# Kernel optimization log

Measured on AMD Instinct MI355X. Metric: run time of the kernel, lower is better.

## Reference

```python
import jax, jax.numpy as jnp
import numpy as np

VOCAB = 32000
EMBED = 1024
HIDDEN = 1024
BATCH = 256
SEQ = 1024


def setup_inputs() -> dict:
    key = jax.random.key(0)
    k1, k2, k3, k4, k5, k6 = jax.random.split(key, 6)
    x = jax.random.randint(k1, (BATCH, SEQ), 0, VOCAB)
    emb = jax.random.normal(k2, (VOCAB, EMBED), dtype=jnp.float32) * 0.02
    # nn.Linear(input_dim, hidden_dim): weight [out, in], bias [out]
    Wi = jax.random.normal(k3, (HIDDEN, EMBED), dtype=jnp.float32) * (1.0 / np.sqrt(EMBED))
    bi = jax.random.normal(k4, (HIDDEN,), dtype=jnp.float32) * 0.01
    Wh = jax.random.normal(k5, (HIDDEN, HIDDEN), dtype=jnp.float32) * (1.0 / np.sqrt(HIDDEN))
    bh = jax.random.normal(k6, (HIDDEN,), dtype=jnp.float32) * 0.01
    return {"x": x, "emb": emb, "Wi": Wi, "bi": bi, "Wh": Wh, "bh": bh}


def reference(x, emb, Wi, bi, Wh, bh):
    # Embed all tokens up front: [B, T, E]
    ex = emb[x]
    # Precompute input projection for every step (batched GEMM): [B, T, H]
    xi = jnp.einsum('bte,he->bth', ex, Wi) + bi
    h0 = jnp.zeros((x.shape[0], Wh.shape[0]), dtype=emb.dtype)

    def step(h, xi_t):  # xi_t: [B, H]
        h_new = jnp.tanh(xi_t + h @ Wh.T + bh)
        return h_new, None

    h_final, _ = jax.lax.scan(step, h0, jnp.swapaxes(xi, 0, 1))  # scan over T
    return h_final  # [B, H]
```

## Files before the change

### kernel.cpp

```cpp
#include <hip/hip_runtime.h>
#include <cmath>

#define BATCHN 256
#define SEQT   1024
#define EMBED  1024
#define HID    1024
#define VOCABN 32000

typedef __attribute__((ext_vector_type(8))) _Float16 half8;
typedef __attribute__((ext_vector_type(4))) _Float16 half4;
typedef __attribute__((ext_vector_type(4))) float    float4v;
typedef __attribute__((ext_vector_type(4))) unsigned int uint4v;

#define LOSCALE 4096.0f
#define LOINV   (1.0f/4096.0f)

union FU16 { _Float16 f; unsigned short u; };
__device__ inline unsigned short f16bits(_Float16 f){ FU16 t; t.f=f; return t.u; }
__device__ inline _Float16 bits16(unsigned short u){ FU16 t; t.u=u; return t.f; }

__device__ inline void async16(const void* g, void* l) {
  __builtin_amdgcn_global_load_lds(
      (const __attribute__((address_space(1))) void*)g,
      (__attribute__((address_space(3))) void*)l, 16, 0, 0);
}

__global__ void convert_f32_f16(const float* __restrict__ in,
                                _Float16* __restrict__ out, int n) {
  int i = (blockIdx.x * blockDim.x + threadIdx.x) * 4;
  if (i + 3 < n) {
    float4v v = *reinterpret_cast<const float4v*>(in + i);
    half4 o;
#pragma unroll
    for (int j = 0; j < 4; ++j) o[j] = (_Float16)v[j];
    *reinterpret_cast<half4*>(out + i) = o;
  }
}

__global__ void split_f32_f16(const float* __restrict__ in,
                              _Float16* __restrict__ hi,
                              _Float16* __restrict__ lo, int n) {
  int i = (blockIdx.x * blockDim.x + threadIdx.x) * 4;
  if (i + 3 < n) {
    float4v v = *reinterpret_cast<const float4v*>(in + i);
    half4 h, l;
#pragma unroll
    for (int j = 0; j < 4; ++j) {
      h[j] = (_Float16)v[j];
      l[j] = (_Float16)((v[j] - (float)h[j]) * LOSCALE);
    }
    *reinterpret_cast<half4*>(hi + i) = h;
    *reinterpret_cast<half4*>(lo + i) = l;
  }
}

__global__ __launch_bounds__(256, 2) void gemm_xi(
    const _Float16* __restrict__ embh,
    const _Float16* __restrict__ Wih,
    const int* __restrict__ x,
    const float* __restrict__ bi,
    _Float16* __restrict__ xi,
    int t0, int Tc)
{
  __shared__ __align__(16) _Float16 As[128 * 64];
  __shared__ __align__(16) _Float16 Bs[128 * 64];
  __shared__ __align__(16) _Float16 stage[128 * 132];
  __shared__ int toks[128];

  const int tid  = threadIdx.x;
  const int wid  = tid >> 6, lane = tid & 63;
  const int nt   = blockIdx.x & 7, mt = blockIdx.x >> 3;
  const int m0   = mt * 128, n0 = nt * 128;

  if (tid < 128) {
    int m  = m0 + tid;
    int tl = m >> 8;
    int b  = m & 255;
    toks[tid] = x[b * SEQT + t0 + tl];
  }
  __syncthreads();

  const _Float16* aptr[4];
  const _Float16* bptr[4];
  int ldsoff[4];
#pragma unroll
  for (int i = 0; i < 4; ++i) {
    int idx = i * 256 + tid;
    int row = idx >> 3, kc = idx & 7;
    aptr[i]   = embh + (size_t)toks[row] * 1024 + kc * 8;
    bptr[i]   = Wih + ((size_t)(n0 + row) << 10) + kc * 8;
    ldsoff[i] = idx * 8;
  }

  float4v acc[4][4] = {};
  const int wm = wid & 1, wn = wid >> 1;
  const int cn = lane & 15, kg = lane >> 4;

  for (int k0 = 0; k0 < 1024; k0 += 64) {
#pragma unroll
    for (int i = 0; i < 4; ++i) {
      async16(aptr[i] + k0, &As[ldsoff[i]]);
      async16(bptr[i] + k0, &Bs[ldsoff[i]]);
    }
    __syncthreads();

    half8 a[4][2], b[4][2];
#pragma unroll
    for (int mf = 0; mf < 4; ++mf)
#pragma unroll
      for (int kf = 0; kf < 2; ++kf)
        a[mf][kf] = *reinterpret_cast<const half8*>(
            &As[(wm * 64 + mf * 16 + cn) * 64 + kf * 32 + kg * 8]);
#pragma unroll
    for (int nf = 0; nf < 4; ++nf)
#pragma unroll
      for (int kf = 0; kf < 2; ++kf)
        b[nf][kf] = *reinterpret_cast<const half8*>(
            &Bs[(wn * 64 + nf * 16 + cn) * 64 + kf * 32 + kg * 8]);

#pragma unroll
    for (int mf = 0; mf < 4; ++mf)
#pragma unroll
      for (int nf = 0; nf < 4; ++nf)
#pragma unroll
        for (int kf = 0; kf < 2; ++kf)
          acc[mf][nf] = __builtin_amdgcn_mfma_f32_16x16x32_f16(
              a[mf][kf], b[nf][kf], acc[mf][nf], 0, 0, 0);
    __syncthreads();
  }

#pragma unroll
  for (int nf = 0; nf < 4; ++nf) {
    int n = wn * 64 + nf * 16 + cn;
    float biv = bi[n0 + n];
#pragma unroll
    for (int mf = 0; mf < 4; ++mf) {
#pragma unroll
      for (int j = 0; j < 4; ++j) {
        int m = wm * 64 + mf * 16 + kg * 4 + j;
        stage[m * 132 + n] = (_Float16)(acc[mf][nf][j] + biv);
      }
    }
  }
  __syncthreads();
#pragma unroll
  for (int p = 0; p < 8; ++p) {
    int chunk = p * 256 + tid;
    int r = chunk >> 4, cc = chunk & 15;
    half4 v0 = *reinterpret_cast<const half4*>(stage + r * 132 + cc * 8);
    half4 v1 = *reinterpret_cast<const half4*>(stage + r * 132 + cc * 8 + 4);
    half8 o;
#pragma unroll
    for (int e = 0; e < 4; ++e) { o[e] = v0[e]; o[4 + e] = v1[e]; }
    int m  = m0 + r;
    int tt = m >> 8, b = m & 255;
    int n  = n0 + cc * 8;
    size_t addr = ((size_t)(tt * 256 + (b >> 4) * 16 + (n >> 6)) << 10)
                + (size_t)((b & 15) * 64 + (n & 63));
    *reinterpret_cast<half8*>(xi + addr) = o;
  }
}

__global__ __launch_bounds__(256, 1) void rnn_scan(
    const _Float16* __restrict__ Whig,
    const _Float16* __restrict__ Wlog,
    const float* __restrict__ bh,
    const _Float16* __restrict__ xi,
    float* __restrict__ hstate,
    float* __restrict__ out,
    _Float16* __restrict__ hexHiA,
    _Float16* __restrict__ hexLoA,
    _Float16* __restrict__ hexHiB,
    _Float16* __restrict__ hexLoB,
    int* __restrict__ bar,
    int t0, int Tc)
{
  __shared__ __align__(16) _Float16 Ahi[16 * 1024];
  __shared__ __align__(16) _Float16 Alo[16 * 1024];
  __shared__ __align__(16) float    part[4 * 64 * 20];

  const int tid  = threadIdx.x;
  const int wv   = tid >> 6, lane = tid & 63;
  const int cn   = lane & 15, kg = lane >> 4;
  const int gb   = blockIdx.x >> 4;
  const int gc   = blockIdx.x & 15;
  const int r0   = gb * 16;
  const int wcol = gc * 64 + wv * 16 + cn;

  half8 whi[32], wlo[32];
#pragma unroll
  for (int c = 0; c < 4; ++c)
#pragma unroll
    for (int kkl = 0; kkl < 8; ++kkl) {
      int col = gc * 64 + c * 16 + cn;
      int k   = (wv * 8 + kkl) * 32 + kg * 8;
      whi[c * 8 + kkl] = *reinterpret_cast<const half8*>(Whig + ((size_t)col << 10) + k);
      wlo[c * 8 + kkl] = *reinterpret_cast<const half8*>(Wlog + ((size_t)col << 10) + k);
    }
  const float bhv = bh[wcol];

  const size_t xibase = ((size_t)(gb * 16 + gc) << 10) + wv * 16 + cn;

  if (t0 == 0) {
#pragma unroll
    for (int p = 0; p < 8; ++p) {
      int idx = p * 256 + tid, row = idx >> 7, cc = idx & 127;
      int bo = (((row << 11) + cc * 16) ^ ((row & 7) << 4));
      half8 z = {0, 0, 0, 0, 0, 0, 0, 0};
      *reinterpret_cast<half8*>(reinterpret_cast<char*>(Ahi) + bo) = z;
      *reinterpret_cast<half8*>(reinterpret_cast<char*>(Alo) + bo) = z;
    }
  } else {
#pragma unroll
    for (int p = 0; p < 8; ++p) {
      int idx = p * 256 + tid, row = idx >> 7, cc = idx & 127;
      const float* hp = hstate + (((size_t)(r0 + row)) << 10) + cc * 8;
      half8 vh, vl;
#pragma unroll
      for (int e = 0; e < 8; ++e) {
        float f = hp[e];
        _Float16 hi = (_Float16)f;
        vh[e] = hi;
        vl[e] = (_Float16)((f - (float)hi) * LOSCALE);
      }
      int bo = (((row << 11) + cc * 16) ^ ((row & 7) << 4));
      *reinterpret_cast<half8*>(reinterpret_cast<char*>(Ahi) + bo) = vh;
      *reinterpret_cast<half8*>(reinterpret_cast<char*>(Alo) + bo) = vl;
    }
  }
  __syncthreads();

  unsigned int xr[4];
#pragma unroll
  for (int j = 0; j < 4; ++j) {
    unsigned long long ap = (unsigned long long)(xi + xibase + (size_t)(kg * 4 + j) * 64);
    asm volatile("global_load_ushort %0, %1, off" : "=v"(xr[j]) : "v"(ap) : "memory");
  }

  uint4v u1h[4], u1l[4];

#define MFMA_Q(K0, K1)                                                          \
  _Pragma("unroll")                                                             \
  for (int kkl = (K0); kkl < (K1); ++kkl) {                                     \
    int ab = (((cn << 11) + (wv * 8 + kkl) * 64 + kg * 16) ^ ((cn & 7) << 4));  \
    half8 ah = *reinterpret_cast<const half8*>(reinterpret_cast<const char*>(Ahi) + ab); \
    half8 al = *reinterpret_cast<const half8*>(reinterpret_cast<const char*>(Alo) + ab); \
    _Pragma("unroll")                                                           \
    for (int c = 0; c < 4; ++c) {                                               \
      asm("v_mfma_f32_16x16x32_f16 %0, %1, %2, %0" : "+v"(ac1[c]) : "v"(ah), "a"(whi[c * 8 + kkl])); \
      asm("v_mfma_f32_16x16x32_f16 %0, %1, %2, %0" : "+v"(ac2[c]) : "v"(al), "a"(whi[c * 8 + kkl])); \
      asm("v_mfma_f32_16x16x32_f16 %0, %1, %2, %0" : "+v"(ac3[c]) : "v"(ah), "a"(wlo[c * 8 + kkl])); \
    }                                                                           \
  }

  for (int tt = 0; tt < Tc; ++tt) {
    float4v ac1[4] = {}, ac2[4] = {}, ac3[4] = {};

    MFMA_Q(0, 4)

    if (tt != 0) {
      asm volatile("s_waitcnt vmcnt(0)" ::: "memory");
      __builtin_amdgcn_sched_barrier(0);
#pragma unroll
      for (int p = 0; p < 4; ++p) {
        int gcbl = 2 + (p >> 1), ch = (p & 1) * 64 + lane;
        int rowl = ch >> 3, c8 = ch & 7;
        int gcb  = wv * 4 + gcbl;
        int bo = (((rowl << 11) + gcb * 128 + c8 * 16) ^ ((rowl & 7) << 4));
        *reinterpret_cast<uint4v*>(reinterpret_cast<char*>(Ahi) + bo) = u1h[p];
        *reinterpret_cast<uint4v*>(reinterpret_cast<char*>(Alo) + bo) = u1l[p];
      }
      asm volatile("s_waitcnt lgkmcnt(0)" ::: "memory");
      __builtin_amdgcn_sched_barrier(0);
    }

    MFMA_Q(4, 8)
    asm volatile("s_nop 7\n\ts_nop 7");

#pragma unroll
    for (int c = 0; c < 4; ++c) {
      float4v pv;
#pragma unroll
      for (int j = 0; j < 4; ++j)
        pv[j] = ac1[c][j] + (ac2[c][j] + ac3[c][j]) * LOINV;
      *reinterpret_cast<float4v*>(&part[(wv * 64 + c * 16 + cn) * 20 + kg * 4]) = pv;
    }
    __syncthreads();

    float4v vs = {};
#pragma unroll
    for (int w = 0; w < 4; ++w) {
      float4v pw = *reinterpret_cast<const float4v*>(
          &part[(w * 64 + wv * 16 + cn) * 20 + kg * 4]);
#pragma unroll
      for (int j = 0; j < 4; ++j) vs[j] += pw[j];
    }
    asm volatile("s_waitcnt vmcnt(0)" ::: "memory");

    const int tglob = t0 + tt;
    const int par = (tt + 1) & 1;
    _Float16* WHi = par ? hexHiA : hexHiB;
    _Float16* WLo = par ? hexLoA : hexLoB;
#pragma unroll
    for (int j = 0; j < 4; ++j) {
      int rowl = kg * 4 + j;
      int row  = r0 + rowl;
      float v = vs[j] + bhv + (float)bits16((unsigned short)xr[j]);
      float ex = __expf(2.0f * v);
      float h  = 1.0f - 2.0f / (ex + 1.0f);
      if (tt < Tc - 1) {
        FU16 thi, tlo;
        thi.f = (_Float16)h;
        tlo.f = (_Float16)((h - (float)thi.f) * LOSCALE);
        size_t off = (((size_t)(gb * 16 + gc)) << 10) + rowl * 64 + wv * 16 + cn;
        asm volatile("global_store_short %0, %1, off sc0 sc1"
                     :: "v"((unsigned long long)(WHi + off)), "v"((unsigned int)thi.u) : "memory");
        asm volatile("global_store_short %0, %1, off sc0 sc1"
                     :: "v"((unsigned long long)(WLo + off)), "v"((unsigned int)tlo.u) : "memory");
      }
      if (tglob == SEQT - 1) out[(((size_t)row) << 10) + wcol] = h;
      else if (tt == Tc - 1) hstate[(((size_t)row) << 10) + wcol] = h;
    }
    if (tt == Tc - 1) break;

    asm volatile("s_waitcnt vmcnt(0)" ::: "memory");
    __builtin_amdgcn_s_barrier();
    const int target = tt + 1;
    if (tid == 0)
      asm volatile("global_store_dword %0, %1, off sc0 sc1"
                   :: "v"((unsigned long long)(bar + (gb * 16 + gc) * 32)),
                      "v"(target) : "memory");

#pragma unroll
    for (int j = 0; j < 4; ++j) {
      unsigned long long ap = (unsigned long long)
          (xi + xibase + (((size_t)(tt + 1)) << 18) + (size_t)(kg * 4 + j) * 64);
      asm volatile("global_load_ushort %0, %1, off" : "=v"(xr[j]) : "v"(ap) : "memory");
    }

    if (tid < 16) {
      const int* fp = bar + (gb * 16 + tid) * 32;
      for (;;) {
        int v;
        asm volatile("global_load_dword %0, %1, off sc0 sc1\n\t"
                     "s_waitcnt vmcnt(0)"
                     : "=v"(v) : "v"((unsigned long long)fp) : "memory");
        if (v >= target) break;
        __builtin_amdgcn_s_sleep(1);
      }
    }
    __builtin_amdgcn_s_barrier();

    const _Float16* SHi = par ? hexHiA : hexHiB;
    const _Float16* SLo = par ? hexLoA : hexLoB;
    uint4v u0h[4], u0l[4];
#pragma unroll
    for (int p = 0; p < 4; ++p) {
      int gcbl = p >> 1, ch = (p & 1) * 64 + lane;
      int rowl = ch >> 3, c8 = ch & 7;
      int gcb  = wv * 4 + gcbl;
      size_t off = (((size_t)(gb * 16 + gcb)) << 10) + rowl * 64 + c8 * 8;
      asm volatile("global_load_dwordx4 %0, %1, off sc0 sc1"
                   : "=v"(u0h[p]) : "v"((unsigned long long)(SHi + off)) : "memory");
      asm volatile("global_load_dwordx4 %0, %1, off sc0 sc1"
                   : "=v"(u0l[p]) : "v"((unsigned long long)(SLo + off)) : "memory");
    }
#pragma unroll
    for (int p = 0; p < 4; ++p) {
      int gcbl = 2 + (p >> 1), ch = (p & 1) * 64 + lane;
      int rowl = ch >> 3, c8 = ch & 7;
      int gcb  = wv * 4 + gcbl;
      size_t off = (((size_t)(gb * 16 + gcb)) << 10) + rowl * 64 + c8 * 8;
      asm volatile("global_load_dwordx4 %0, %1, off sc0 sc1"
                   : "=v"(u1h[p]) : "v"((unsigned long long)(SHi + off)) : "memory");
      asm volatile("global_load_dwordx4 %0, %1, off sc0 sc1"
                   : "=v"(u1l[p]) : "v"((unsigned long long)(SLo + off)) : "memory");
    }
    asm volatile("s_waitcnt vmcnt(8)" ::: "memory");
    __builtin_amdgcn_sched_barrier(0);
#pragma unroll
    for (int p = 0; p < 4; ++p) {
      int gcbl = p >> 1, ch = (p & 1) * 64 + lane;
      int rowl = ch >> 3, c8 = ch & 7;
      int gcb  = wv * 4 + gcbl;
      int bo = (((rowl << 11) + gcb * 128 + c8 * 16) ^ ((rowl & 7) << 4));
      *reinterpret_cast<uint4v*>(reinterpret_cast<char*>(Ahi) + bo) = u0h[p];
      *reinterpret_cast<uint4v*>(reinterpret_cast<char*>(Alo) + bo) = u0l[p];
    }
    asm volatile("s_waitcnt lgkmcnt(0)" ::: "memory");
    __builtin_amdgcn_sched_barrier(0);
  }
#undef MFMA_Q
}

extern "C" void kernel_launch(void* const* d_in, const int* in_sizes, int n_in,
                              void* d_out, int out_size, void* d_ws, size_t ws_size,
                              hipStream_t stream) {
  const int*   x   = (const int*)  d_in[0];
  const float* emb = (const float*)d_in[1];
  const float* Wi  = (const float*)d_in[2];
  const float* bi  = (const float*)d_in[3];
  const float* Wh  = (const float*)d_in[4];
  const float* bh  = (const float*)d_in[5];
  float* out = (float*)d_out;

  char* ws = (char*)d_ws;
  size_t off = 0;
  auto alloc = [&](size_t bytes) -> void* {
    void* p = ws + off;
    off = (off + bytes + 255) & ~(size_t)255;
    return p;
  };

  _Float16* embh   = (_Float16*)alloc((size_t)VOCABN * EMBED * 2);
  _Float16* Wih    = (_Float16*)alloc((size_t)HID * EMBED * 2);
  _Float16* Whih   = (_Float16*)alloc((size_t)HID * HID * 2);
  _Float16* Wloh   = (_Float16*)alloc((size_t)HID * HID * 2);
  float*    hstate = (float*)   alloc((size_t)BATCHN * HID * 4);
  _Float16* hexHiA = (_Float16*)alloc((size_t)BATCHN * HID * 2);
  _Float16* hexLoA = (_Float16*)alloc((size_t)BATCHN * HID * 2);
  _Float16* hexHiB = (_Float16*)alloc((size_t)BATCHN * HID * 2);
  _Float16* hexLoB = (_Float16*)alloc((size_t)BATCHN * HID * 2);
  int* bar  = (int*)alloc(256 * 32 * 4);
  size_t fixed = off;

  int Tc = 1024;
  while (Tc > 4 && fixed + (size_t)BATCHN * Tc * HID * 2 > ws_size) Tc >>= 1;
  _Float16* xih = (_Float16*)alloc((size_t)BATCHN * Tc * HID * 2);

  {
    int n = VOCABN * EMBED;
    convert_f32_f16<<<n / 1024, 256, 0, stream>>>(emb, embh, n);
    n = HID * EMBED;
    convert_f32_f16<<<n / 1024, 256, 0, stream>>>(Wi, Wih, n);
    n = HID * HID;
    split_f32_f16<<<n / 1024, 256, 0, stream>>>(Wh, Whih, Wloh, n);
  }

  for (int t0 = 0; t0 < SEQT; t0 += Tc) {
    int grid = (BATCHN * Tc / 128) * 8;
    gemm_xi<<<grid, 256, 0, stream>>>(embh, Wih, x, bi, xih, t0, Tc);
    hipMemsetAsync(bar, 0, 256 * 32 * 4, stream);
    rnn_scan<<<256, 256, 0, stream>>>(Whih, Wloh, bh, xih, hstate, out,
                                      hexHiA, hexLoA, hexHiB, hexLoB, bar, t0, Tc);
  }
}
```

Measured before the change: 5.018 ms.

## Use per-wave flags and triple-buffered exchange to drop block barriers in RNN scan

Replaces the per-block flag and the two s_barrier calls around the inter-block handshake with per-wavefront flags. Each wave now signals and polls only the producer waves whose columns it needs. The hidden-state exchange buffers go from double to triple buffering so waves can run ahead without overwriting data still being read. The epilogue is also remapped so each lane handles four contiguous columns, which makes the xi loads, exchange stores and output stores vectorized. This adds more flag traffic and polling lanes in exchange for less block-wide synchronization.

```diff
diff --git a/kernel.cpp b/kernel.cpp
--- a/kernel.cpp
+++ b/kernel.cpp
@@ -11,6 +11,7 @@
 typedef __attribute__((ext_vector_type(4))) _Float16 half4;
 typedef __attribute__((ext_vector_type(4))) float    float4v;
 typedef __attribute__((ext_vector_type(4))) unsigned int uint4v;
+typedef __attribute__((ext_vector_type(2))) unsigned int uint2v;
 
 #define LOSCALE 4096.0f
 #define LOINV   (1.0f/4096.0f)
@@ -168,16 +169,15 @@
     const _Float16* __restrict__ xi,
     float* __restrict__ hstate,
     float* __restrict__ out,
-    _Float16* __restrict__ hexHiA,
-    _Float16* __restrict__ hexLoA,
-    _Float16* __restrict__ hexHiB,
-    _Float16* __restrict__ hexLoB,
-    int* __restrict__ bar,
+    _Float16* __restrict__ hx0, _Float16* __restrict__ lx0,
+    _Float16* __restrict__ hx1, _Float16* __restrict__ lx1,
+    _Float16* __restrict__ hx2, _Float16* __restrict__ lx2,
+    int* __restrict__ flags,
     int t0, int Tc)
 {
   __shared__ __align__(16) _Float16 Ahi[16 * 1024];
   __shared__ __align__(16) _Float16 Alo[16 * 1024];
-  __shared__ __align__(16) float    part[4 * 64 * 20];
+  __shared__ __align__(16) float    part[2][4][16][68];
 
   const int tid  = threadIdx.x;
   const int wv   = tid >> 6, lane = tid & 63;
@@ -185,7 +185,10 @@
   const int gb   = blockIdx.x >> 4;
   const int gc   = blockIdx.x & 15;
   const int r0   = gb * 16;
-  const int wcol = gc * 64 + wv * 16 + cn;
+  const int rowl = lane & 15;
+  const int cib  = wv * 16 + ((lane >> 4) << 2);
+  const int gcol = gc * 64 + cib;
+  const size_t blockbase = ((size_t)(gb * 16 + gc)) << 10;
 
   half8 whi[32], wlo[32];
 #pragma unroll
@@ -197,9 +200,7 @@
       whi[c * 8 + kkl] = *reinterpret_cast<const half8*>(Whig + ((size_t)col << 10) + k);
       wlo[c * 8 + kkl] = *reinterpret_cast<const half8*>(Wlog + ((size_t)col << 10) + k);
     }
-  const float bhv = bh[wcol];
-
-  const size_t xibase = ((size_t)(gb * 16 + gc) << 10) + wv * 16 + cn;
+  const float4v bh4 = *reinterpret_cast<const float4v*>(bh + gcol);
 
   if (t0 == 0) {
 #pragma unroll
@@ -230,11 +231,13 @@
   }
   __syncthreads();
 
-  unsigned int xr[4];
-#pragma unroll
-  for (int j = 0; j < 4; ++j) {
-    unsigned long long ap = (unsigned long long)(xi + xibase + (size_t)(kg * 4 + j) * 64);
-    asm volatile("global_load_ushort %0, %1, off" : "=v"(xr[j]) : "v"(ap) : "memory");
+  _Float16 *cH = hx0, *cL = lx0, *nH = hx1, *nL = lx1, *oH = hx2, *oL = lx2;
+
+  uint2v xr;
+  {
+    unsigned long long ap = (unsigned long long)
+        (xi + blockbase + (size_t)(rowl * 64 + cib));
+    asm volatile("global_load_dwordx2 %0, %1, off" : "=v"(xr) : "v"(ap) : "memory");
   }
 
   uint4v u1h[4], u1l[4];
@@ -254,6 +257,7 @@
   }
 
   for (int tt = 0; tt < Tc; ++tt) {
+    const int pb = tt & 1;
     float4v ac1[4] = {}, ac2[4] = {}, ac3[4] = {};
 
     MFMA_Q(0, 4)
@@ -264,9 +268,9 @@
 #pragma unroll
       for (int p = 0; p < 4; ++p) {
         int gcbl = 2 + (p >> 1), ch = (p & 1) * 64 + lane;
-        int rowl = ch >> 3, c8 = ch & 7;
-        int gcb  = wv * 4 + gcbl;
-        int bo = (((rowl << 11) + gcb * 128 + c8 * 16) ^ ((rowl & 7) << 4));
+        int rw = ch >> 3, c8 = ch & 7;
+        int gcb = wv * 4 + gcbl;
+        int bo = (((rw << 11) + gcb * 128 + c8 * 16) ^ ((rw & 7) << 4));
         *reinterpret_cast<uint4v*>(reinterpret_cast<char*>(Ahi) + bo) = u1h[p];
         *reinterpret_cast<uint4v*>(reinterpret_cast<char*>(Alo) + bo) = u1l[p];
       }
@@ -278,68 +282,75 @@
     asm volatile("s_nop 7\n\ts_nop 7");
 
 #pragma unroll
-    for (int c = 0; c < 4; ++c) {
-      float4v pv;
+    for (int c = 0; c < 4; ++c)
 #pragma unroll
       for (int j = 0; j < 4; ++j)
-        pv[j] = ac1[c][j] + (ac2[c][j] + ac3[c][j]) * LOINV;
-      *reinterpret_cast<float4v*>(&part[(wv * 64 + c * 16 + cn) * 20 + kg * 4]) = pv;
-    }
+        part[pb][wv][kg * 4 + j][c * 16 + cn] =
+            ac1[c][j] + (ac2[c][j] + ac3[c][j]) * LOINV;
     __syncthreads();
 
     float4v vs = {};
 #pragma unroll
     for (int w = 0; w < 4; ++w) {
-      float4v pw = *reinterpret_cast<const float4v*>(
-          &part[(w * 64 + wv * 16 + cn) * 20 + kg * 4]);
+      float4v pw = *reinterpret_cast<const float4v*>(&part[pb][w][rowl][cib]);
 #pragma unroll
       for (int j = 0; j < 4; ++j) vs[j] += pw[j];
     }
     asm volatile("s_waitcnt vmcnt(0)" ::: "memory");
 
     const int tglob = t0 + tt;
-    const int par = (tt + 1) & 1;
-    _Float16* WHi = par ? hexHiA : hexHiB;
-    _Float16* WLo = par ? hexLoA : hexLoB;
-#pragma unroll
-    for (int j = 0; j < 4; ++j) {
-      int rowl = kg * 4 + j;
-      int row  = r0 + rowl;
-      float v = vs[j] + bhv + (float)bits16((unsigned short)xr[j]);
+    float hv[4];
+    unsigned short hu[4], lu[4];
+#pragma unroll
+    for (int cj = 0; cj < 4; ++cj) {
+      unsigned int w = (cj < 2) ? xr[0] : xr[1];
+      unsigned short xb = (cj & 1) ? (unsigned short)(w >> 16) : (unsigned short)(w & 0xffffu);
+      float v = vs[cj] + bh4[cj] + (float)bits16(xb);
       float ex = __expf(2.0f * v);
       float h  = 1.0f - 2.0f / (ex + 1.0f);
-      if (tt < Tc - 1) {
-        FU16 thi, tlo;
-        thi.f = (_Float16)h;
-        tlo.f = (_Float16)((h - (float)thi.f) * LOSCALE);
-        size_t off = (((size_t)(gb * 16 + gc)) << 10) + rowl * 64 + wv * 16 + cn;
-        asm volatile("global_store_short %0, %1, off sc0 sc1"
-                     :: "v"((unsigned long long)(WHi + off)), "v"((unsigned int)thi.u) : "memory");
-        asm volatile("global_store_short %0, %1, off sc0 sc1"
-                     :: "v"((unsigned long long)(WLo + off)), "v"((unsigned int)tlo.u) : "memory");
-      }
-      if (tglob == SEQT - 1) out[(((size_t)row) << 10) + wcol] = h;
-      else if (tt == Tc - 1) hstate[(((size_t)row) << 10) + wcol] = h;
+      hv[cj] = h;
+      FU16 thi, tlo;
+      thi.f = (_Float16)h;
+      tlo.f = (_Float16)((h - (float)thi.f) * LOSCALE);
+      hu[cj] = thi.u; lu[cj] = tlo.u;
+    }
+    if (tt < Tc - 1) {
+      uint2v ph, pl;
+      ph[0] = (unsigned int)hu[0] | ((unsigned int)hu[1] << 16);
+      ph[1] = (unsigned int)hu[2] | ((unsigned int)hu[3] << 16);
+      pl[0] = (unsigned int)lu[0] | ((unsigned int)lu[1] << 16);
+      pl[1] = (unsigned int)lu[2] | ((unsigned int)lu[3] << 16);
+      size_t off = blockbase + (size_t)(rowl * 64 + cib);
+      asm volatile("global_store_dwordx2 %0, %1, off sc0 sc1"
+                   :: "v"((unsigned long long)(cH + off)), "v"(ph) : "memory");
+      asm volatile("global_store_dwordx2 %0, %1, off sc0 sc1"
+                   :: "v"((unsigned long long)(cL + off)), "v"(pl) : "memory");
+    }
+    if (tglob == SEQT - 1) {
+      float4v o = {hv[0], hv[1], hv[2], hv[3]};
+      *reinterpret_cast<float4v*>(out + (((size_t)(r0 + rowl)) << 10) + gcol) = o;
+    } else if (tt == Tc - 1) {
+      float4v o = {hv[0], hv[1], hv[2], hv[3]};
+      *reinterpret_cast<float4v*>(hstate + (((size_t)(r0 + rowl)) << 10) + gcol) = o;
     }
     if (tt == Tc - 1) break;
 
     asm volatile("s_waitcnt vmcnt(0)" ::: "memory");
-    __builtin_amdgcn_s_barrier();
     const int target = tt + 1;
-    if (tid == 0)
+    if (lane == 0)
       asm volatile("global_store_dword %0, %1, off sc0 sc1"
-                   :: "v"((unsigned long long)(bar + (gb * 16 + gc) * 32)),
+                   :: "v"((unsigned long long)(flags + ((gb * 16 + gc) * 4 + wv) * 32)),
                       "v"(target) : "memory");
 
-#pragma unroll
-    for (int j = 0; j < 4; ++j) {
+    {
       unsigned long long ap = (unsigned long long)
-          (xi + xibase + (((size_t)(tt + 1)) << 18) + (size_t)(kg * 4 + j) * 64);
-      asm volatile("global_load_ushort %0, %1, off" : "=v"(xr[j]) : "v"(ap) : "memory");
-    }
-
-    if (tid < 16) {
-      const int* fp = bar + (gb * 16 + tid) * 32;
+          (xi + blockbase + (((size_t)(tt + 1)) << 18) + (size_t)(rowl * 64 + cib));
+      asm volatile("global_load_dwordx2 %0, %1, off" : "=v"(xr) : "v"(ap) : "memory");
+    }
+
+    if (lane < 16) {
+      int pgc = wv * 4 + (lane >> 2), pwv = lane & 3;
+      const int* fp = flags + ((gb * 16 + pgc) * 4 + pwv) * 32;
       for (;;) {
         int v;
         asm volatile("global_load_dword %0, %1, off sc0 sc1\n\t"
@@ -349,46 +360,46 @@
         __builtin_amdgcn_s_sleep(1);
       }
     }
-    __builtin_amdgcn_s_barrier();
-
-    const _Float16* SHi = par ? hexHiA : hexHiB;
-    const _Float16* SLo = par ? hexLoA : hexLoB;
+
     uint4v u0h[4], u0l[4];
 #pragma unroll
     for (int p = 0; p < 4; ++p) {
       int gcbl = p >> 1, ch = (p & 1) * 64 + lane;
-      int rowl = ch >> 3, c8 = ch & 7;
-      int gcb  = wv * 4 + gcbl;
-      size_t off = (((size_t)(gb * 16 + gcb)) << 10) + rowl * 64 + c8 * 8;
+      int rw = ch >> 3, c8 = ch & 7;
+      int gcb = wv * 4 + gcbl;
+      size_t off = (((size_t)(gb * 16 + gcb)) << 10) + rw * 64 + c8 * 8;
       asm volatile("global_load_dwordx4 %0, %1, off sc0 sc1"
-                   : "=v"(u0h[p]) : "v"((unsigned long long)(SHi + off)) : "memory");
+                   : "=v"(u0h[p]) : "v"((unsigned long long)(cH + off)) : "memory");
       asm volatile("global_load_dwordx4 %0, %1, off sc0 sc1"
-                   : "=v"(u0l[p]) : "v"((unsigned long long)(SLo + off)) : "memory");
+                   : "=v"(u0l[p]) : "v"((unsigned long long)(cL + off)) : "memory");
     }
 #pragma unroll
     for (int p = 0; p < 4; ++p) {
       int gcbl = 2 + (p >> 1), ch = (p & 1) * 64 + lane;
-      int rowl = ch >> 3, c8 = ch & 7;
-      int gcb  = wv * 4 + gcbl;
-      size_t off = (((size_t)(gb * 16 + gcb)) << 10) + rowl * 64 + c8 * 8;
+      int rw = ch >> 3, c8 = ch & 7;
+      int gcb = wv * 4 + gcbl;
+      size_t off = (((size_t)(gb * 16 + gcb)) << 10) + rw * 64 + c8 * 8;
       asm volatile("global_load_dwordx4 %0, %1, off sc0 sc1"
-                   : "=v"(u1h[p]) : "v"((unsigned long long)(SHi + off)) : "memory");
+                   : "=v"(u1h[p]) : "v"((unsigned long long)(cH + off)) : "memory");
       asm volatile("global_load_dwordx4 %0, %1, off sc0 sc1"
-                   : "=v"(u1l[p]) : "v"((unsigned long long)(SLo + off)) : "memory");
+                   : "=v"(u1l[p]) : "v"((unsigned long long)(cL + off)) : "memory");
     }
     asm volatile("s_waitcnt vmcnt(8)" ::: "memory");
     __builtin_amdgcn_sched_barrier(0);
 #pragma unroll
     for (int p = 0; p < 4; ++p) {
       int gcbl = p >> 1, ch = (p & 1) * 64 + lane;
-      int rowl = ch >> 3, c8 = ch & 7;
-      int gcb  = wv * 4 + gcbl;
-      int bo = (((rowl << 11) + gcb * 128 + c8 * 16) ^ ((rowl & 7) << 4));
+      int rw = ch >> 3, c8 = ch & 7;
+      int gcb = wv * 4 + gcbl;
+      int bo = (((rw << 11) + gcb * 128 + c8 * 16) ^ ((rw & 7) << 4));
       *reinterpret_cast<uint4v*>(reinterpret_cast<char*>(Ahi) + bo) = u0h[p];
       *reinterpret_cast<uint4v*>(reinterpret_cast<char*>(Alo) + bo) = u0l[p];
     }
     asm volatile("s_waitcnt lgkmcnt(0)" ::: "memory");
     __builtin_amdgcn_sched_barrier(0);
+
+    _Float16* th = cH; cH = nH; nH = oH; oH = th;
+    _Float16* tl = cL; cL = nL; nL = oL; oL = tl;
   }
 #undef MFMA_Q
 }
@@ -417,11 +428,13 @@
   _Float16* Whih   = (_Float16*)alloc((size_t)HID * HID * 2);
   _Float16* Wloh   = (_Float16*)alloc((size_t)HID * HID * 2);
   float*    hstate = (float*)   alloc((size_t)BATCHN * HID * 4);
-  _Float16* hexHiA = (_Float16*)alloc((size_t)BATCHN * HID * 2);
-  _Float16* hexLoA = (_Float16*)alloc((size_t)BATCHN * HID * 2);
-  _Float16* hexHiB = (_Float16*)alloc((size_t)BATCHN * HID * 2);
-  _Float16* hexLoB = (_Float16*)alloc((size_t)BATCHN * HID * 2);
-  int* bar  = (int*)alloc(256 * 32 * 4);
+  _Float16* hx0 = (_Float16*)alloc((size_t)BATCHN * HID * 2);
+  _Float16* lx0 = (_Float16*)alloc((size_t)BATCHN * HID * 2);
+  _Float16* hx1 = (_Float16*)alloc((size_t)BATCHN * HID * 2);
+  _Float16* lx1 = (_Float16*)alloc((size_t)BATCHN * HID * 2);
+  _Float16* hx2 = (_Float16*)alloc((size_t)BATCHN * HID * 2);
+  _Float16* lx2 = (_Float16*)alloc((size_t)BATCHN * HID * 2);
+  int* flags = (int*)alloc(16 * 16 * 4 * 32 * 4);
   size_t fixed = off;
 
   int Tc = 1024;
@@ -440,8 +453,8 @@
   for (int t0 = 0; t0 < SEQT; t0 += Tc) {
     int grid = (BATCHN * Tc / 128) * 8;
     gemm_xi<<<grid, 256, 0, stream>>>(embh, Wih, x, bi, xih, t0, Tc);
-    hipMemsetAsync(bar, 0, 256 * 32 * 4, stream);
+    hipMemsetAsync(flags, 0, 16 * 16 * 4 * 32 * 4, stream);
     rnn_scan<<<256, 256, 0, stream>>>(Whih, Wloh, bh, xih, hstate, out,
-                                      hexHiA, hexLoA, hexHiB, hexLoB, bar, t0, Tc);
-  }
-}
+                                      hx0, lx0, hx1, lx1, hx2, lx2, flags, t0, Tc);
+  }
+}
```

Result: slower. 5.704 ms (+13.7%).
